# Optimization experiments

Hardware: AMD Instinct MI355X
Metric: run time of the kernel (lower is better)

## Reference

```python
import jax, jax.numpy as jnp
import numpy as np

B, L, C = 512, 2048, 32  # batch, seq_len, num_labels


def setup_inputs() -> dict:
    key = jax.random.key(0)
    k1, k2, k3 = jax.random.split(key, 3)
    emissions = jax.random.normal(k1, (B, L, C), dtype=jnp.float32)
    tags = jax.random.randint(k2, (B, L), 0, C, dtype=jnp.int32)
    mask = jnp.ones((B, L), dtype=jnp.int32)
    # learned parameter: transitions (num_labels, num_labels)
    transitions = jax.random.normal(k3, (C, C), dtype=jnp.float32)
    return {"emissions": emissions, "transitions": transitions, "tags": tags, "mask": mask}


def _crf_nll(emissions, transitions, tags, mask):
    Bn, Ln, Cn = emissions.shape
    maskf = mask.astype(emissions.dtype)

    # ---- gold-path score (vectorized over the t loop) ----
    # emit[b,t] = emissions[b,t,tags[b,t]] for t in [0, L-2]
    emit = jnp.take_along_axis(emissions[:, : Ln - 1], tags[:, : Ln - 1, None], axis=2)[..., 0]
    # trans[b,t] = transitions[tags[b,t], tags[b,t+1]]
    trans = transitions[tags[:, : Ln - 1], tags[:, 1:]]
    score = jnp.sum(emit * maskf[:, : Ln - 1] + trans * maskf[:, 1:], axis=1)

    msum = jnp.sum(mask, axis=1)
    last_idx = jnp.clip(msum - 1, 0)  # index of last valid tag
    last_tag = jnp.take_along_axis(tags, last_idx[:, None], axis=1)[:, 0]
    le_t = jnp.clip(msum, 1) - 1
    last_emission = emissions[jnp.arange(Bn), le_t, last_tag]
    score = score + last_emission

    # ---- log-partition via forward algorithm (lax.scan over time) ----
    # Faithful to source: alpha_t[b,n,p] = alpha[b,p] + transitions[n,p] + emit[b,n],
    # reduced over p; the source's mask line is an algebraic no-op (a*m + a*(1-m) = a).
    def step(alpha, emit_t):
        # alpha: (B, C) over prev label p; emit_t: (B, C) over next label n
        alpha_new = jax.nn.logsumexp(alpha[:, None, :] + transitions[None, :, :], axis=2) + emit_t
        return alpha_new, None

    alpha0 = emissions[:, 0]                      # (B, C)
    em_rest = jnp.swapaxes(emissions[:, 1:], 0, 1)  # (L-1, B, C)
    alpha, _ = jax.lax.scan(step, alpha0, em_rest)
    log_Z = jax.nn.logsumexp(alpha, axis=1)       # (B,)

    return jnp.mean(log_Z - score)


def reference(emissions, transitions, tags, mask):
    return _crf_nll(emissions, transitions, tags, mask)
```

## Files before the change

kernel.cpp:

```cpp
#include <hip/hip_runtime.h>
#include <stdint.h>

typedef short bf16x8 __attribute__((ext_vector_type(8)));
typedef float f32x16 __attribute__((ext_vector_type(16)));

#define LOG2E 1.44269504088896340736f
#define LN2f  0.69314718055994530942f

constexpr int Bn = 512;
constexpr int Ln = 2048;
constexpr int Cn = 32;
constexpr int NSEG = 32;
constexpr int SEGLEN = 64;
constexpr int WARM = 16;
constexpr int NGRP = 16;

__device__ __forceinline__ uint32_t pack2_bf16(float lo, float hi) {
    uint32_t a = __float_as_uint(lo) + 0x8000u;
    uint32_t b = __float_as_uint(hi) + 0x8000u;
    return __builtin_amdgcn_perm(b, a, 0x07060302u);
}

__global__ __launch_bounds__(64, 1) void crf_scan(
    const float* __restrict__ emis, const float* __restrict__ trans,
    float* __restrict__ dDelta)
{
    const int lane = threadIdx.x;
    const int h    = lane >> 5;
    const int bl   = lane & 31;
    const int g    = blockIdx.x & (NGRP - 1);
    const int s    = blockIdx.x >> 4;
    const int b    = g * 32 + bl;
    const size_t eb = (size_t)b * Ln * Cn;

    bf16x8 A1, A2;
    {
        float e1[8], e2[8];
        #pragma unroll
        for (int j = 0; j < 8; ++j) {
            int c1 = 4 * h + (j & 3) + 8 * (j >> 2);
            e1[j] = __expf(trans[bl * Cn + c1]);
            e2[j] = __expf(trans[bl * Cn + c1 + 16]);
        }
        union { uint32_t u[4]; bf16x8 v; } ua, ub;
        #pragma unroll
        for (int q = 0; q < 4; ++q) {
            ua.u[q] = pack2_bf16(e1[2*q], e1[2*q+1]);
            ub.u[q] = pack2_bf16(e2[2*q], e2[2*q+1]);
        }
        A1 = ua.v; A2 = ub.v;
    }

    const f32x16 zeroC = {0.f,0.f,0.f,0.f,0.f,0.f,0.f,0.f,0.f,0.f,0.f,0.f,0.f,0.f,0.f,0.f};

    f32x16 Dv;
    bf16x8 B1, B2;
    float offF = 0.f;
    float adj  = 0.f;
    float4 buf[8][4];

    const int t0 = (s == 0) ? 0 : s * SEGLEN - WARM;

    auto loadEm = [&](int t, float4 (&dst)[4]) {
        const float4* p = (const float4*)(emis + eb + (size_t)t * Cn + 4 * h);
        dst[0] = p[0]; dst[1] = p[2]; dst[2] = p[4]; dst[3] = p[6];
    };

    auto packB = [&]() {
        union { uint32_t u[4]; bf16x8 v; } p1, p2;
        #pragma unroll
        for (int q = 0; q < 4; ++q) {
            p1.u[q] = pack2_bf16(Dv[2*q],     Dv[2*q + 1]);
            p2.u[q] = pack2_bf16(Dv[8 + 2*q], Dv[8 + 2*q + 1]);
        }
        B1 = p1.v; B2 = p2.v;
    };

    auto initStep = [&](const float4 (&bu)[4]) {
        #pragma unroll
        for (int q = 0; q < 4; ++q) {
            Dv[4*q+0] = __expf(bu[q].x);
            Dv[4*q+1] = __expf(bu[q].y);
            Dv[4*q+2] = __expf(bu[q].z);
            Dv[4*q+3] = __expf(bu[q].w);
        }
        packB();
    };

    auto stepMfma = [&](const float4 (&bu)[4], float a) {
        f32x16 acc = __builtin_amdgcn_mfma_f32_32x32x16_bf16(A1, B1, zeroC, 0, 0, 0);
        acc = __builtin_amdgcn_mfma_f32_32x32x16_bf16(A2, B2, acc, 0, 0, 0);
        #pragma unroll
        for (int q = 0; q < 4; ++q) {
            float x0 = exp2f(fmaf(bu[q].x, LOG2E, a));
            float x1 = exp2f(fmaf(bu[q].y, LOG2E, a));
            float x2 = exp2f(fmaf(bu[q].z, LOG2E, a));
            float x3 = exp2f(fmaf(bu[q].w, LOG2E, a));
            Dv[4*q+0] = acc[4*q+0] * x0;
            Dv[4*q+1] = acc[4*q+1] * x1;
            Dv[4*q+2] = acc[4*q+2] * x2;
            Dv[4*q+3] = acc[4*q+3] * x3;
        }
        packB();
    };

    auto renorm = [&]() {
        float m0 = fmaxf(fmaxf(Dv[0], Dv[1]),  fmaxf(Dv[2],  Dv[3]));
        float m1 = fmaxf(fmaxf(Dv[4], Dv[5]),  fmaxf(Dv[6],  Dv[7]));
        float m2 = fmaxf(fmaxf(Dv[8], Dv[9]),  fmaxf(Dv[10], Dv[11]));
        float m3 = fmaxf(fmaxf(Dv[12],Dv[13]), fmaxf(Dv[14], Dv[15]));
        float m  = fmaxf(fmaxf(m0, m1), fmaxf(m2, m3));
        m = fmaxf(m, __shfl_xor(m, 32, 64));
        int k = (int)((__float_as_uint(m) >> 23) & 0xffu) - 126;
        offF += (float)k * LN2f;
        adj = -(float)k;
    };

    auto sumD = [&]() {
        float t = 0.f;
        #pragma unroll
        for (int r = 0; r < 16; ++r) t += Dv[r];
        t += __shfl_xor(t, 32, 64);
        return t;
    };

    #pragma unroll
    for (int u = 0; u < 8; ++u) loadEm(t0 + u, buf[u]);

    initStep(buf[0]);
    loadEm(t0 + 8, buf[0]);
    #pragma unroll
    for (int u = 1; u < 8; ++u) {
        stepMfma(buf[u], 0.f);
        loadEm(t0 + 8 + u, buf[u]);
    }
    renorm();

    int nblk, tb;
    if (s == 0) {
        nblk = 7;
        tb = 8;
    } else {
        #pragma unroll
        for (int u = 0; u < 8; ++u) {
            stepMfma(buf[u], (u == 0) ? adj : 0.f);
            loadEm(t0 + 16 + u, buf[u]);
        }
        adj = 0.f;
        float S = sumD();
        adj = -__log2f(S);
        offF = 0.f;
        nblk = 8;
        tb = s * SEGLEN;
    }

    #pragma unroll 1
    for (int blk = 0; blk < nblk; ++blk) {
        #pragma unroll
        for (int u = 0; u < 8; ++u) {
            stepMfma(buf[u], (u == 0) ? adj : 0.f);
            loadEm(min(tb + u + 8, Ln - 1), buf[u]);
        }
        adj = 0.f;
        if (blk < nblk - 1) renorm();
        tb += 8;
    }

    float delta = offF + __logf(sumD());
    if (lane < 32) dDelta[s * Bn + b] = delta;
}

__global__ __launch_bounds__(256) void crf_score(
    const float* __restrict__ emis, const float* __restrict__ trans,
    const int* __restrict__ tags, const int* __restrict__ mask,
    float* __restrict__ dScore)
{
    __shared__ float Tl[Cn * Cn];
    __shared__ float sred[4];
    __shared__ int   mred[4];
    const int b   = blockIdx.x;
    const int tid = threadIdx.x;
    for (int i = tid; i < Cn * Cn; i += 256) Tl[i] = trans[i];
    __syncthreads();

    const size_t tB = (size_t)b * Ln;
    const size_t eB = (size_t)b * Ln * Cn;
    float sc = 0.f;
    int   ms = 0;
    #pragma unroll
    for (int k = 0; k < Ln / 256; ++k) {
        int t  = tid + k * 256;
        int tg = tags[tB + t];
        int mk = mask[tB + t];
        ms += mk;
        if (t < Ln - 1) {
            int tg1 = tags[tB + t + 1];
            int mk1 = mask[tB + t + 1];
            sc += (float)mk  * emis[eB + (size_t)t * Cn + tg];
            sc += (float)mk1 * Tl[(tg << 5) + tg1];
        }
    }
    #pragma unroll
    for (int o = 32; o > 0; o >>= 1) {
        sc += __shfl_down(sc, o, 64);
        ms += __shfl_down(ms, o, 64);
    }
    if ((tid & 63) == 0) { sred[tid >> 6] = sc; mred[tid >> 6] = ms; }
    __syncthreads();
    if (tid == 0) {
        float S = 0.f; int M = 0;
        #pragma unroll
        for (int w = 0; w < 4; ++w) { S += sred[w]; M += mred[w]; }
        int last_idx = max(M - 1, 0);
        int le_t     = max(M, 1) - 1;
        int lt = tags[tB + last_idx];
        float le = emis[(tB + le_t) * Cn + lt];
        dScore[b] = S + le;
    }
}

__global__ void crf_final(const float* __restrict__ dDelta,
                          const float* __restrict__ dScore,
                          float* __restrict__ out)
{
    __shared__ float red[8];
    int b = threadIdx.x;
    float lz = 0.f;
    #pragma unroll
    for (int s2 = 0; s2 < NSEG; ++s2) lz += dDelta[s2 * Bn + b];
    float val = lz - dScore[b];
    #pragma unroll
    for (int o = 32; o > 0; o >>= 1) val += __shfl_down(val, o, 64);
    if ((b & 63) == 0) red[b >> 6] = val;
    __syncthreads();
    if (b == 0) {
        float t = 0.f;
        #pragma unroll
        for (int w = 0; w < 8; ++w) t += red[w];
        out[0] = t * (1.0f / (float)Bn);
    }
}

extern "C" void kernel_launch(void* const* d_in, const int* in_sizes, int n_in,
                              void* d_out, int out_size, void* d_ws, size_t ws_size,
                              hipStream_t stream)
{
    const float* emis  = (const float*)d_in[0];
    const float* trans = (const float*)d_in[1];
    const int*   tags  = (const int*)d_in[2];
    const int*   mask  = (const int*)d_in[3];
    float* wsf = (float*)d_ws;
    float* dDelta = wsf;
    float* dScore = wsf + NSEG * Bn;
    crf_scan <<<NGRP * NSEG, 64, 0, stream>>>(emis, trans, dDelta);
    crf_score<<<Bn, 256, 0, stream>>>(emis, trans, tags, mask, dScore);
    crf_final<<<1, Bn, 0, stream>>>(dDelta, dScore, (float*)d_out);
}
```

Before: 232.9 us.

## Stage emission tiles through swizzled LDS with coalesced cooperative loads

Replaces the per-lane strided float4 emission loads with a cooperative scheme. The whole wavefront loads 8-timestep tiles for all 32 batch rows with contiguous float4 reads, then writes them into double-buffered LDS using an XOR swizzle, and each lane reads back its 16 values per step. The aim is to make global reads coalesced and hide latency by prefetching two tiles ahead. The cost is more LDS traffic, 32 float4 registers of staging, and write/read interleaving inside the serial step loop, which may lengthen the critical path.

```diff
diff --git a/kernel.cpp b/kernel.cpp
--- a/kernel.cpp
+++ b/kernel.cpp
@@ -12,8 +12,8 @@
 constexpr int Cn = 32;
 constexpr int NSEG = 32;
 constexpr int SEGLEN = 64;
-constexpr int WARM = 16;
 constexpr int NGRP = 16;
+constexpr int TS = 8;
 
 __device__ __forceinline__ uint32_t pack2_bf16(float lo, float hi) {
     uint32_t a = __float_as_uint(lo) + 0x8000u;
@@ -25,13 +25,18 @@
     const float* __restrict__ emis, const float* __restrict__ trans,
     float* __restrict__ dDelta)
 {
+    __shared__ float lds[2][TS * Cn * Cn];
     const int lane = threadIdx.x;
     const int h    = lane >> 5;
     const int bl   = lane & 31;
     const int g    = blockIdx.x & (NGRP - 1);
     const int s    = blockIdx.x >> 4;
-    const int b    = g * 32 + bl;
-    const size_t eb = (size_t)b * Ln * Cn;
+    const size_t ebg = (size_t)(g * 32) * Ln * Cn;
+
+    const int wt   = lane >> 3;
+    const int wc   = lane & 7;
+    const int wswz = (wt + (wc << 3)) & 31;
+    const int wrow = (wt * Cn + 4 * wc) * Cn;
 
     bf16x8 A1, A2;
     {
@@ -57,13 +62,31 @@
     bf16x8 B1, B2;
     float offF = 0.f;
     float adj  = 0.f;
-    float4 buf[8][4];
-
-    const int t0 = (s == 0) ? 0 : s * SEGLEN - WARM;
-
-    auto loadEm = [&](int t, float4 (&dst)[4]) {
-        const float4* p = (const float4*)(emis + eb + (size_t)t * Cn + 4 * h);
-        dst[0] = p[0]; dst[1] = p[2]; dst[2] = p[4]; dst[3] = p[6];
+    float4 G[32];
+
+    const int t0 = (s == 0) ? 0 : s * SEGLEN - 2 * TS;
+
+    auto loadRound = [&](int j, int r) {
+        int T = min(t0 + TS * j, Ln - TS);
+        G[r] = *(const float4*)(emis + ebg + (size_t)r * Ln * Cn + (size_t)T * Cn + 4 * lane);
+    };
+    auto writeRound = [&](int bi, int r) {
+        float* L = lds[bi];
+        int col = r ^ wswz;
+        L[wrow          + col] = G[r].x;
+        L[wrow +   Cn   + col] = G[r].y;
+        L[wrow + 2*Cn   + col] = G[r].z;
+        L[wrow + 3*Cn   + col] = G[r].w;
+    };
+    auto read16 = [&](int bi, int tl, float (&E)[16]) {
+        const float* L = lds[bi];
+        #pragma unroll
+        for (int q = 0; q < 4; ++q) {
+            int swz  = (tl + ((2*q + h) << 3)) & 31;
+            int base = (tl * Cn + 8*q + 4*h) * Cn + (bl ^ swz);
+            #pragma unroll
+            for (int i = 0; i < 4; ++i) E[4*q + i] = L[base + i * Cn];
+        }
     };
 
     auto packB = [&]() {
@@ -76,31 +99,18 @@
         B1 = p1.v; B2 = p2.v;
     };
 
-    auto initStep = [&](const float4 (&bu)[4]) {
-        #pragma unroll
-        for (int q = 0; q < 4; ++q) {
-            Dv[4*q+0] = __expf(bu[q].x);
-            Dv[4*q+1] = __expf(bu[q].y);
-            Dv[4*q+2] = __expf(bu[q].z);
-            Dv[4*q+3] = __expf(bu[q].w);
-        }
+    auto initStep = [&](const float (&E)[16]) {
+        #pragma unroll
+        for (int r = 0; r < 16; ++r) Dv[r] = __expf(E[r]);
         packB();
     };
 
-    auto stepMfma = [&](const float4 (&bu)[4], float a) {
+    auto stepMfma = [&](const float (&E)[16], float a) {
         f32x16 acc = __builtin_amdgcn_mfma_f32_32x32x16_bf16(A1, B1, zeroC, 0, 0, 0);
         acc = __builtin_amdgcn_mfma_f32_32x32x16_bf16(A2, B2, acc, 0, 0, 0);
         #pragma unroll
-        for (int q = 0; q < 4; ++q) {
-            float x0 = exp2f(fmaf(bu[q].x, LOG2E, a));
-            float x1 = exp2f(fmaf(bu[q].y, LOG2E, a));
-            float x2 = exp2f(fmaf(bu[q].z, LOG2E, a));
-            float x3 = exp2f(fmaf(bu[q].w, LOG2E, a));
-            Dv[4*q+0] = acc[4*q+0] * x0;
-            Dv[4*q+1] = acc[4*q+1] * x1;
-            Dv[4*q+2] = acc[4*q+2] * x2;
-            Dv[4*q+3] = acc[4*q+3] * x3;
-        }
+        for (int r = 0; r < 16; ++r)
+            Dv[r] = acc[r] * exp2f(fmaf(E[r], LOG2E, a));
         packB();
     };
 
@@ -124,50 +134,47 @@
         return t;
     };
 
-    #pragma unroll
-    for (int u = 0; u < 8; ++u) loadEm(t0 + u, buf[u]);
-
-    initStep(buf[0]);
-    loadEm(t0 + 8, buf[0]);
-    #pragma unroll
-    for (int u = 1; u < 8; ++u) {
-        stepMfma(buf[u], 0.f);
-        loadEm(t0 + 8 + u, buf[u]);
-    }
-    renorm();
-
-    int nblk, tb;
-    if (s == 0) {
-        nblk = 7;
-        tb = 8;
-    } else {
-        #pragma unroll
-        for (int u = 0; u < 8; ++u) {
-            stepMfma(buf[u], (u == 0) ? adj : 0.f);
-            loadEm(t0 + 16 + u, buf[u]);
+    auto doTile = [&](int k, bool firstInit) {
+        const int bi = k & 1;
+        #pragma unroll
+        for (int u = 0; u < TS; ++u) {
+            float E[16];
+            read16(bi, u, E);
+            if (u < 4) {
+                #pragma unroll
+                for (int v = 0; v < 8; ++v) writeRound(bi ^ 1, u * 8 + v);
+            } else {
+                #pragma unroll
+                for (int v = 0; v < 8; ++v) loadRound(k + 2, (u - 4) * 8 + v);
+            }
+            if (u == 0 && firstInit) initStep(E);
+            else                     stepMfma(E, (u == 0) ? adj : 0.f);
         }
         adj = 0.f;
-        float S = sumD();
-        adj = -__log2f(S);
-        offF = 0.f;
-        nblk = 8;
-        tb = s * SEGLEN;
-    }
-
+    };
+
+    #pragma unroll
+    for (int r = 0; r < 32; ++r) loadRound(0, r);
+    #pragma unroll
+    for (int r = 0; r < 32; ++r) writeRound(0, r);
+    #pragma unroll
+    for (int r = 0; r < 32; ++r) loadRound(1, r);
+
+    const int ntiles = (s == 0) ? 8 : 10;
     #pragma unroll 1
-    for (int blk = 0; blk < nblk; ++blk) {
-        #pragma unroll
-        for (int u = 0; u < 8; ++u) {
-            stepMfma(buf[u], (u == 0) ? adj : 0.f);
-            loadEm(min(tb + u + 8, Ln - 1), buf[u]);
-        }
-        adj = 0.f;
-        if (blk < nblk - 1) renorm();
-        tb += 8;
+    for (int k = 0; k < ntiles; ++k) {
+        doTile(k, k == 0);
+        if (s > 0 && k == 1) {
+            float S = sumD();
+            adj  = -__log2f(S);
+            offF = 0.f;
+        } else if (k < ntiles - 1) {
+            renorm();
+        }
     }
 
     float delta = offF + __logf(sumD());
-    if (lane < 32) dDelta[s * Bn + b] = delta;
+    if (lane < 32) dDelta[s * Bn + g * 32 + bl] = delta;
 }
 
 __global__ __launch_bounds__(256) void crf_score(
```

After: 237.8 us. +2.1%, slower.
